# Performance work log

Measured on AMD Instinct MI355X. Metric: run time of the kernel, lower is better.

The kernel has to match this reference:

```python
import jax, jax.numpy as jnp
import numpy as np

ORDER, POINTS, N = 3, 16, 2048
D1, D2, POOL1, POOL2, LABELS = 64, 32, 32, 8, 10


def setup_inputs() -> dict:
    key = jax.random.key(0)
    ks = jax.random.split(key, 8)
    adj = jax.random.uniform(ks[0], (ORDER, N, N), dtype=jnp.float32)  # normalized adjacency powers
    # original inits weight_matrix uniform(-1000, 1000)
    wm = jax.random.uniform(ks[1], (ORDER, POINTS), dtype=jnp.float32, minval=-1000.0, maxval=1000.0)
    w1 = jax.random.normal(ks[2], (ORDER * POINTS, D1), dtype=jnp.float32) * 0.1
    b1 = jnp.zeros((D1,), jnp.float32)
    w2 = jax.random.normal(ks[3], (D1, D2), dtype=jnp.float32) * 0.1
    b2 = jnp.zeros((D2,), jnp.float32)
    p1 = jax.random.normal(ks[4], (D2, POOL1), dtype=jnp.float32) * 0.1
    pb1 = jnp.zeros((POOL1,), jnp.float32)
    p2 = jax.random.normal(ks[5], (POOL1, POOL2), dtype=jnp.float32) * 0.1
    pb2 = jnp.zeros((POOL2,), jnp.float32)
    cw = jax.random.normal(ks[6], (POOL2 * D2, LABELS), dtype=jnp.float32) * 0.1
    cb = jnp.zeros((LABELS,), jnp.float32)
    return dict(adj=adj, wm=wm, w1=w1, b1=b1, w2=w2, b2=b2,
                p1=p1, pb1=pb1, p2=p2, pb2=pb2, cw=cw, cb=cb)


def reference(adj, wm, w1, b1, w2, b2, p1, pb1, p2, pb2, cw, cb):
    order, n, _ = adj.shape
    pts = wm.shape[1]
    # LearningToEvaluateLayer: per-order outer product theta ⊗ A, cos, mean over last node dim
    # scores: [order, pts, n, n]; feats: [order, pts, n]
    feats = jnp.mean(jnp.cos(wm[:, :, None, None] * adj[:, None, :, :]), axis=3)
    # torch.t(features) per order then cat along dim=1 -> [n, order*pts]
    ms = jnp.transpose(feats, (2, 0, 1)).reshape(n, order * pts)
    h1 = jax.nn.relu(ms @ w1 + b1)          # [n, D1]
    h2 = jax.nn.relu(h1 @ w2 + b2)          # [n, D2]
    # SagePoolingLayer: attention over nodes (softmax along dim=0)
    abstract = jnp.tanh(h2 @ p1 + pb1)      # [n, POOL1]
    att = jax.nn.softmax(abstract @ p2 + pb2, axis=0)  # [n, POOL2]
    g = (att.T @ h2).reshape(1, -1)         # [1, POOL2*D2]
    logits = g @ cw + cb                    # [1, LABELS]
    return jax.nn.log_softmax(logits, axis=1)
```

## Files before the change

### kernel.cpp

```cpp
#include <hip/hip_runtime.h>
#include <hip/hip_bf16.h>
#include <math.h>

#define ORDER  3
#define POINTS 16
#define NNODES 2048
#define D1 64
#define D2 32
#define POOL1 32
#define POOL2 8
#define LABELS 10

__global__ __launch_bounds__(64) void k_feats(const float* __restrict__ adj,
                                              const float* __restrict__ wm,
                                              float* __restrict__ ms) {
    const int i    = blockIdx.x;
    const int o    = blockIdx.y;
    const int lane = threadIdx.x;

    const float INV2PI = 0.15915494309189535f;
    float wr[POINTS];
#pragma unroll
    for (int p = 0; p < POINTS; ++p)
        wr[p] = wm[o * POINTS + p] * INV2PI;

    const float4* row4 =
        reinterpret_cast<const float4*>(adj + ((size_t)o * NNODES + (size_t)i) * NNODES);

    float acc[POINTS];
#pragma unroll
    for (int p = 0; p < POINTS; ++p) acc[p] = 0.0f;

#pragma unroll
    for (int c = 0; c < NNODES / (4 * 64); ++c) {
        float4 a4 = row4[c * 64 + lane];
        float av[4] = {a4.x, a4.y, a4.z, a4.w};
#pragma unroll
        for (int e = 0; e < 4; ++e) {
            float a = av[e];
#pragma unroll
            for (int p = 0; p < POINTS; ++p) {
                float r = __builtin_amdgcn_fractf(a * wr[p]);
                acc[p] += __builtin_amdgcn_cosf(r);
            }
        }
    }

#pragma unroll
    for (int p = 0; p < POINTS; ++p) {
        float v = acc[p];
#pragma unroll
        for (int off = 32; off >= 1; off >>= 1)
            v += __shfl_xor(v, off, 64);
        acc[p] = v;
    }

    if (lane == 0) {
        float* out = ms + (size_t)i * (ORDER * POINTS) + o * POINTS;
        const float rn = 1.0f / (float)NNODES;
#pragma unroll
        for (int p = 0; p < POINTS; ++p)
            out[p] = acc[p] * rn;
    }
}

__global__ __launch_bounds__(256) void k_mlp(const float* __restrict__ ms,
                                             const float* __restrict__ w1,
                                             const float* __restrict__ b1,
                                             const float* __restrict__ w2,
                                             const float* __restrict__ b2,
                                             const float* __restrict__ p1,
                                             const float* __restrict__ pb1,
                                             const float* __restrict__ p2,
                                             const float* __restrict__ pb2,
                                             float* __restrict__ h2out,
                                             float* __restrict__ sout) {
    const int t  = threadIdx.x;
    const int r0 = blockIdx.x * 32;

    __shared__ float lms[32 * 48];
    __shared__ float lw1[48 * D1];
    __shared__ float lh1[32 * D1];
    __shared__ float lw2[D1 * D2];
    __shared__ float lh2[32 * D2];
    __shared__ float lp1[D2 * POOL1];
    __shared__ float lav[32 * POOL1];
    __shared__ float lp2[POOL1 * POOL2];
    __shared__ float ls[32 * POOL2];
    __shared__ float lb1[D1], lb2[D2], lpb1[POOL1], lpb2[POOL2];

    for (int idx = t; idx < 32 * 48; idx += 256) lms[idx] = ms[(size_t)r0 * 48 + idx];
    for (int idx = t; idx < 48 * D1; idx += 256) lw1[idx] = w1[idx];
    for (int idx = t; idx < D1 * D2; idx += 256) lw2[idx] = w2[idx];
    for (int idx = t; idx < D2 * POOL1; idx += 256) lp1[idx] = p1[idx];
    if (t < POOL1 * POOL2) lp2[t] = p2[t];
    if (t < D1) lb1[t] = b1[t];
    if (t < D2) lb2[t] = b2[t];
    if (t < POOL1) lpb1[t] = pb1[t];
    if (t < POOL2) lpb2[t] = pb2[t];
    __syncthreads();

    {
        const int dim = t & 63;
        const int rg  = t >> 6;
        float acc[8];
#pragma unroll
        for (int j = 0; j < 8; ++j) acc[j] = 0.0f;
#pragma unroll
        for (int k4 = 0; k4 < 12; ++k4) {
            const float wa = lw1[(k4 * 4 + 0) * D1 + dim];
            const float wb = lw1[(k4 * 4 + 1) * D1 + dim];
            const float wc = lw1[(k4 * 4 + 2) * D1 + dim];
            const float wd = lw1[(k4 * 4 + 3) * D1 + dim];
#pragma unroll
            for (int j = 0; j < 8; ++j) {
                const float4 m4 = *reinterpret_cast<const float4*>(&lms[(rg * 8 + j) * 48 + k4 * 4]);
                acc[j] = fmaf(m4.x, wa, fmaf(m4.y, wb, fmaf(m4.z, wc, fmaf(m4.w, wd, acc[j]))));
            }
        }
        const float bb = lb1[dim];
#pragma unroll
        for (int j = 0; j < 8; ++j)
            lh1[(rg * 8 + j) * D1 + dim] = fmaxf(acc[j] + bb, 0.0f);
    }
    __syncthreads();

    {
        const int dim = t & 31;
        const int rg  = t >> 5;
        float acc[4] = {0.0f, 0.0f, 0.0f, 0.0f};
#pragma unroll
        for (int k4 = 0; k4 < 16; ++k4) {
            const float wa = lw2[(k4 * 4 + 0) * D2 + dim];
            const float wb = lw2[(k4 * 4 + 1) * D2 + dim];
            const float wc = lw2[(k4 * 4 + 2) * D2 + dim];
            const float wd = lw2[(k4 * 4 + 3) * D2 + dim];
#pragma unroll
            for (int j = 0; j < 4; ++j) {
                const float4 h4 = *reinterpret_cast<const float4*>(&lh1[(rg * 4 + j) * D1 + k4 * 4]);
                acc[j] = fmaf(h4.x, wa, fmaf(h4.y, wb, fmaf(h4.z, wc, fmaf(h4.w, wd, acc[j]))));
            }
        }
        const float bb = lb2[dim];
#pragma unroll
        for (int j = 0; j < 4; ++j)
            lh2[(rg * 4 + j) * D2 + dim] = fmaxf(acc[j] + bb, 0.0f);
    }
    __syncthreads();

    reinterpret_cast<float4*>(h2out)[(size_t)blockIdx.x * 256 + t] =
        reinterpret_cast<const float4*>(lh2)[t];

    {
        const int dim = t & 31;
        const int rg  = t >> 5;
        float acc[4] = {0.0f, 0.0f, 0.0f, 0.0f};
#pragma unroll
        for (int k4 = 0; k4 < 8; ++k4) {
            const float wa = lp1[(k4 * 4 + 0) * POOL1 + dim];
            const float wb = lp1[(k4 * 4 + 1) * POOL1 + dim];
            const float wc = lp1[(k4 * 4 + 2) * POOL1 + dim];
            const float wd = lp1[(k4 * 4 + 3) * POOL1 + dim];
#pragma unroll
            for (int j = 0; j < 4; ++j) {
                const float4 h4 = *reinterpret_cast<const float4*>(&lh2[(rg * 4 + j) * D2 + k4 * 4]);
                acc[j] = fmaf(h4.x, wa, fmaf(h4.y, wb, fmaf(h4.z, wc, fmaf(h4.w, wd, acc[j]))));
            }
        }
        const float bb = lpb1[dim];
#pragma unroll
        for (int j = 0; j < 4; ++j)
            lav[(rg * 4 + j) * POOL1 + dim] = tanhf(acc[j] + bb);
    }
    __syncthreads();

    {
        const int row = t >> 3;
        const int c   = t & 7;
        float acc = lpb2[c];
#pragma unroll
        for (int k = 0; k < POOL1; ++k)
            acc = fmaf(lav[row * POOL1 + k], lp2[k * POOL2 + c], acc);
        ls[row * POOL2 + c] = acc;
    }
    __syncthreads();

    sout[(size_t)r0 * POOL2 + t] = ls[t];
}

__global__ __launch_bounds__(256) void k_pool(const float* __restrict__ sIn,
                                              const float* __restrict__ h2,
                                              float* __restrict__ g) {
    const int c = blockIdx.x;
    const int t = threadIdx.x;

    __shared__ float attc[NNODES];
    __shared__ float red[16];
    __shared__ float4 pp[32][8];

    float pm = -1e30f;
    for (int r = t; r < NNODES; r += 256)
        pm = fmaxf(pm, sIn[(size_t)r * POOL2 + c]);
#pragma unroll
    for (int off = 32; off >= 1; off >>= 1)
        pm = fmaxf(pm, __shfl_xor(pm, off, 64));
    if ((t & 63) == 0) red[t >> 6] = pm;
    __syncthreads();
    const float mx = fmaxf(fmaxf(red[0], red[1]), fmaxf(red[2], red[3]));

    float ps = 0.0f;
    for (int r = t; r < NNODES; r += 256) {
        float e = expf(sIn[(size_t)r * POOL2 + c] - mx);
        attc[r] = e;
        ps += e;
    }
#pragma unroll
    for (int off = 32; off >= 1; off >>= 1)
        ps += __shfl_xor(ps, off, 64);
    if ((t & 63) == 0) red[8 + (t >> 6)] = ps;
    __syncthreads();
    const float rinv = 1.0f / (red[8] + red[9] + red[10] + red[11]);

    const int d4  = t & 7;
    const int seg = t >> 3;
    float4 acc = make_float4(0.f, 0.f, 0.f, 0.f);
    const float4* h2v = reinterpret_cast<const float4*>(h2);
    for (int j = 0; j < 64; ++j) {
        const int r = seg * 64 + ((j + seg * 8) & 63);
        const float a = attc[r];
        const float4 h = h2v[(size_t)r * 8 + d4];
        acc.x = fmaf(a, h.x, acc.x);
        acc.y = fmaf(a, h.y, acc.y);
        acc.z = fmaf(a, h.z, acc.z);
        acc.w = fmaf(a, h.w, acc.w);
    }
    pp[seg][d4] = acc;
    __syncthreads();
    if (t < 8) {
        float4 s = make_float4(0.f, 0.f, 0.f, 0.f);
#pragma unroll
        for (int sg = 0; sg < 32; ++sg) {
            const float4 v = pp[sg][t];
            s.x += v.x; s.y += v.y; s.z += v.z; s.w += v.w;
        }
        s.x *= rinv; s.y *= rinv; s.z *= rinv; s.w *= rinv;
        reinterpret_cast<float4*>(g)[c * 8 + t] = s;
    }
}

__global__ __launch_bounds__(640) void k_logits(const float* __restrict__ g,
                                                const float* __restrict__ cw,
                                                const float* __restrict__ cb,
                                                float* __restrict__ out) {
    const int l    = threadIdx.x >> 6;
    const int lane = threadIdx.x & 63;
    __shared__ float lg[LABELS];

    float p = 0.0f;
    for (int k = lane; k < POOL2 * D2; k += 64)
        p = fmaf(g[k], cw[(size_t)k * LABELS + l], p);
#pragma unroll
    for (int off = 32; off >= 1; off >>= 1)
        p += __shfl_xor(p, off, 64);
    if (lane == 0) lg[l] = p + cb[l];
    __syncthreads();
    if (threadIdx.x == 0) {
        float m = lg[0];
#pragma unroll
        for (int i = 1; i < LABELS; ++i) m = fmaxf(m, lg[i]);
        float se = 0.0f;
#pragma unroll
        for (int i = 0; i < LABELS; ++i) se += expf(lg[i] - m);
        const float lse = m + logf(se);
#pragma unroll
        for (int i = 0; i < LABELS; ++i) out[i] = lg[i] - lse;
    }
}

extern "C" void kernel_launch(void* const* d_in, const int* in_sizes, int n_in,
                              void* d_out, int out_size, void* d_ws, size_t ws_size,
                              hipStream_t stream) {
    const float* adj = (const float*)d_in[0];
    const float* wm  = (const float*)d_in[1];
    const float* w1  = (const float*)d_in[2];
    const float* b1  = (const float*)d_in[3];
    const float* w2  = (const float*)d_in[4];
    const float* b2  = (const float*)d_in[5];
    const float* p1  = (const float*)d_in[6];
    const float* pb1 = (const float*)d_in[7];
    const float* p2  = (const float*)d_in[8];
    const float* pb2 = (const float*)d_in[9];
    const float* cw  = (const float*)d_in[10];
    const float* cb  = (const float*)d_in[11];
    float* out = (float*)d_out;

    float* ws = (float*)d_ws;
    float* ms  = ws;
    float* h2  = ms + (size_t)NNODES * ORDER * POINTS;
    float* sS  = h2 + (size_t)NNODES * D2;
    float* g   = sS + (size_t)NNODES * POOL2;

    hipLaunchKernelGGL(k_feats, dim3(NNODES, ORDER), dim3(64), 0, stream, adj, wm, ms);
    hipLaunchKernelGGL(k_mlp, dim3(NNODES / 32), dim3(256), 0, stream,
                       ms, w1, b1, w2, b2, p1, pb1, p2, pb2, h2, sS);
    hipLaunchKernelGGL(k_pool, dim3(POOL2), dim3(256), 0, stream, sS, h2, g);
    hipLaunchKernelGGL(k_logits, dim3(1), dim3(640), 0, stream, g, cw, cb, out);
}
```

Measured before the change: 148.0 us.

## Split attention pooling across node blocks with partial sums reduced in logits kernel

The pooling kernel now launches 32 blocks, one per 64-node slice, instead of 8 blocks (one per attention column). Each block recomputes the global column max and sum over all nodes redundantly and then computes its slice's attention-weighted h2 partial for all 8 columns. The logits kernel reduces the 32 partials and applies the normalizer. This raises parallelism in a small tail kernel at the cost of each block redundantly reading the full score matrix twice.

```diff
diff --git a/kernel.cpp b/kernel.cpp
--- a/kernel.cpp
+++ b/kernel.cpp
@@ -10,6 +10,7 @@
 #define POOL1 32
 #define POOL2 8
 #define LABELS 10
+#define PBLK   32
 
 __global__ __launch_bounds__(64) void k_feats(const float* __restrict__ adj,
                                               const float* __restrict__ wm,
@@ -190,75 +191,85 @@
 
 __global__ __launch_bounds__(256) void k_pool(const float* __restrict__ sIn,
                                               const float* __restrict__ h2,
-                                              float* __restrict__ g) {
-    const int c = blockIdx.x;
+                                              float* __restrict__ part,
+                                              float* __restrict__ rinvOut) {
+    const int b = blockIdx.x;
     const int t = threadIdx.x;
 
-    __shared__ float attc[NNODES];
-    __shared__ float red[16];
-    __shared__ float4 pp[32][8];
+    __shared__ float red[256];
+    __shared__ float colmax[POOL2];
+    __shared__ float colsum[POOL2];
+    __shared__ float att_l[64 * POOL2];
+
+    const int c  = t & 7;
+    const int rg = t >> 3;
 
     float pm = -1e30f;
-    for (int r = t; r < NNODES; r += 256)
-        pm = fmaxf(pm, sIn[(size_t)r * POOL2 + c]);
-#pragma unroll
-    for (int off = 32; off >= 1; off >>= 1)
-        pm = fmaxf(pm, __shfl_xor(pm, off, 64));
-    if ((t & 63) == 0) red[t >> 6] = pm;
-    __syncthreads();
-    const float mx = fmaxf(fmaxf(red[0], red[1]), fmaxf(red[2], red[3]));
-
+    for (int j = 0; j < 64; ++j)
+        pm = fmaxf(pm, sIn[(size_t)(rg * 64 + j) * POOL2 + c]);
+    red[c * 32 + rg] = pm;
+    __syncthreads();
+    if (t < POOL2) {
+        float m = red[t * 32];
+#pragma unroll
+        for (int k = 1; k < 32; ++k) m = fmaxf(m, red[t * 32 + k]);
+        colmax[t] = m;
+    }
+    __syncthreads();
+
+    const float mx = colmax[c];
     float ps = 0.0f;
-    for (int r = t; r < NNODES; r += 256) {
-        float e = expf(sIn[(size_t)r * POOL2 + c] - mx);
-        attc[r] = e;
-        ps += e;
-    }
-#pragma unroll
-    for (int off = 32; off >= 1; off >>= 1)
-        ps += __shfl_xor(ps, off, 64);
-    if ((t & 63) == 0) red[8 + (t >> 6)] = ps;
-    __syncthreads();
-    const float rinv = 1.0f / (red[8] + red[9] + red[10] + red[11]);
-
-    const int d4  = t & 7;
-    const int seg = t >> 3;
-    float4 acc = make_float4(0.f, 0.f, 0.f, 0.f);
-    const float4* h2v = reinterpret_cast<const float4*>(h2);
-    for (int j = 0; j < 64; ++j) {
-        const int r = seg * 64 + ((j + seg * 8) & 63);
-        const float a = attc[r];
-        const float4 h = h2v[(size_t)r * 8 + d4];
-        acc.x = fmaf(a, h.x, acc.x);
-        acc.y = fmaf(a, h.y, acc.y);
-        acc.z = fmaf(a, h.z, acc.z);
-        acc.w = fmaf(a, h.w, acc.w);
-    }
-    pp[seg][d4] = acc;
-    __syncthreads();
-    if (t < 8) {
-        float4 s = make_float4(0.f, 0.f, 0.f, 0.f);
-#pragma unroll
-        for (int sg = 0; sg < 32; ++sg) {
-            const float4 v = pp[sg][t];
-            s.x += v.x; s.y += v.y; s.z += v.z; s.w += v.w;
-        }
-        s.x *= rinv; s.y *= rinv; s.z *= rinv; s.w *= rinv;
-        reinterpret_cast<float4*>(g)[c * 8 + t] = s;
-    }
-}
-
-__global__ __launch_bounds__(640) void k_logits(const float* __restrict__ g,
+    for (int j = 0; j < 64; ++j)
+        ps += expf(sIn[(size_t)(rg * 64 + j) * POOL2 + c] - mx);
+    red[c * 32 + rg] = ps;
+    __syncthreads();
+    if (t < POOL2) {
+        float s = 0.0f;
+#pragma unroll
+        for (int k = 0; k < 32; ++k) s += red[t * 32 + k];
+        colsum[t] = s;
+        if (b == 0) rinvOut[t] = 1.0f / s;
+    }
+    __syncthreads();
+
+    for (int idx = t; idx < 64 * POOL2; idx += 256) {
+        const int j  = idx >> 3;
+        const int cc = idx & 7;
+        att_l[idx] = expf(sIn[(size_t)(b * 64 + j) * POOL2 + cc] - colmax[cc]);
+    }
+    __syncthreads();
+
+    {
+        const int c2 = t >> 5;
+        const int d  = t & 31;
+        float acc = 0.0f;
+        for (int j = 0; j < 64; ++j)
+            acc = fmaf(att_l[j * POOL2 + c2], h2[(size_t)(b * 64 + j) * D2 + d], acc);
+        part[(size_t)b * 256 + t] = acc;
+    }
+}
+
+__global__ __launch_bounds__(640) void k_logits(const float* __restrict__ part,
+                                                const float* __restrict__ rinv8,
                                                 const float* __restrict__ cw,
                                                 const float* __restrict__ cb,
                                                 float* __restrict__ out) {
     const int l    = threadIdx.x >> 6;
     const int lane = threadIdx.x & 63;
+    __shared__ float gs[256];
     __shared__ float lg[LABELS];
+
+    if (threadIdx.x < 256) {
+        float s = 0.0f;
+#pragma unroll
+        for (int b = 0; b < PBLK; ++b) s += part[(size_t)b * 256 + threadIdx.x];
+        gs[threadIdx.x] = s * rinv8[threadIdx.x >> 5];
+    }
+    __syncthreads();
 
     float p = 0.0f;
     for (int k = lane; k < POOL2 * D2; k += 64)
-        p = fmaf(g[k], cw[(size_t)k * LABELS + l], p);
+        p = fmaf(gs[k], cw[(size_t)k * LABELS + l], p);
 #pragma unroll
     for (int off = 32; off >= 1; off >>= 1)
         p += __shfl_xor(p, off, 64);
@@ -294,15 +305,16 @@
     const float* cb  = (const float*)d_in[11];
     float* out = (float*)d_out;
 
-    float* ws = (float*)d_ws;
-    float* ms  = ws;
-    float* h2  = ms + (size_t)NNODES * ORDER * POINTS;
-    float* sS  = h2 + (size_t)NNODES * D2;
-    float* g   = sS + (size_t)NNODES * POOL2;
+    float* ws   = (float*)d_ws;
+    float* ms   = ws;
+    float* h2   = ms + (size_t)NNODES * ORDER * POINTS;
+    float* sS   = h2 + (size_t)NNODES * D2;
+    float* part = sS + (size_t)NNODES * POOL2;
+    float* rinv = part + (size_t)PBLK * 256;
 
     hipLaunchKernelGGL(k_feats, dim3(NNODES, ORDER), dim3(64), 0, stream, adj, wm, ms);
     hipLaunchKernelGGL(k_mlp, dim3(NNODES / 32), dim3(256), 0, stream,
                        ms, w1, b1, w2, b2, p1, pb1, p2, pb2, h2, sS);
-    hipLaunchKernelGGL(k_pool, dim3(POOL2), dim3(256), 0, stream, sS, h2, g);
-    hipLaunchKernelGGL(k_logits, dim3(1), dim3(640), 0, stream, g, cw, cb, out);
-}
+    hipLaunchKernelGGL(k_pool, dim3(PBLK), dim3(256), 0, stream, sS, h2, part, rinv);
+    hipLaunchKernelGGL(k_logits, dim3(1), dim3(640), 0, stream, part, rinv, cw, cb, out);
+}
```

After: 152.0 us. 2.7% more time.
